# Kernel tuning notes

Measured on AMD Instinct MI355X. Metric: run time of the kernel, lower is better.

Reference implementation:

```python
import jax, jax.numpy as jnp
import numpy as np

K = 8               # top-k frequencies
PRED_LEN = 96       # prediction_length
LOW_FREQ = 1        # low_frequency cutoff (drops DC)


def setup_inputs() -> dict:
    key = jax.random.key(0)
    x = jax.random.normal(key, (32, 2048, 64), dtype=jnp.float32)
    return {"x": x}


def reference(x):
    b, t, d = x.shape
    x_freq = jnp.fft.rfft(x, axis=1)                 # (b, t//2+1, d) complex
    freqs = jnp.fft.rfftfreq(t).astype(x.dtype)
    if t % 2 == 0:
        x_freq = x_freq[:, LOW_FREQ:-1]              # drop DC and Nyquist
        f = freqs[LOW_FREQ:-1]
    else:
        x_freq = x_freq[:, LOW_FREQ:]
        f = freqs[LOW_FREQ:]

    # top-k over frequency dim (axis=1), independently per (b, d)
    mag = jnp.abs(x_freq)                            # (b, F, d)
    _, idx = jax.lax.top_k(jnp.moveaxis(mag, 1, 2), K)  # (b, d, K), sorted desc
    idx = jnp.moveaxis(idx, 1, 2)                    # (b, K, d)
    x_k = jnp.take_along_axis(x_freq, idx, axis=1)   # (b, K, d) complex
    f_k = f[idx]                                     # (b, K, d)

    # extrapolate: add conjugate (negative) frequencies, then cos-sum
    x2 = jnp.concatenate([x_k, jnp.conj(x_k)], axis=1)  # (b, 2K, d)
    f2 = jnp.concatenate([f_k, -f_k], axis=1)           # (b, 2K, d)
    t_val = jnp.arange(t + PRED_LEN, dtype=x.dtype)     # (T,)
    amp = jnp.abs(x2) / t                               # (b, 2K, d)
    phase = jnp.angle(x2)                               # (b, 2K, d)
    # (b, 2K, T, d) broadcast intermediate, reduced over freq axis
    x_time = amp[:, :, None, :] * jnp.cos(
        2.0 * np.float32(np.pi) * f2[:, :, None, :] * t_val[None, None, :, None]
        + phase[:, :, None, :]
    )
    return x_time.sum(axis=1)                        # (b, t+PRED_LEN, d)
```

## Files before the change

### kernel.cpp

```cpp
#include <hip/hip_runtime.h>
#include <math.h>

#define BB 32
#define TT 2048
#define DD 64
#define PRED 96
#define TP (TT + PRED)
#define KTOP 8
#define MARGIN 1e-4f
#define PI_D 3.14159265358979323846

__device__ __forceinline__ int br6(int l) { return (int)(__brev((unsigned)l) >> 26); }
static constexpr int BR4[16] = {0,8,4,12,2,10,6,14,1,9,5,13,3,11,7,15};
static constexpr float C32T[16] = {
    1.0f, 0.98078528040323044913f, 0.92387953251128675613f, 0.83146961230254523708f,
    0.70710678118654752440f, 0.55557023301960222474f, 0.38268343236508977173f, 0.19509032201612826785f,
    0.0f, -0.19509032201612826785f, -0.38268343236508977173f, -0.55557023301960222474f,
    -0.70710678118654752440f, -0.83146961230254523708f, -0.92387953251128675613f, -0.98078528040323044913f};
static constexpr float S32T[16] = {
    0.0f, 0.19509032201612826785f, 0.38268343236508977173f, 0.55557023301960222474f,
    0.70710678118654752440f, 0.83146961230254523708f, 0.92387953251128675613f, 0.98078528040323044913f,
    1.0f, 0.98078528040323044913f, 0.92387953251128675613f, 0.83146961230254523708f,
    0.70710678118654752440f, 0.55557023301960222474f, 0.38268343236508977173f, 0.19509032201612826785f};

__device__ __forceinline__ float2 ctw(float2 a, int m) {
    const float rev = (float)m * (1.0f / 2048.0f);
    const float c = __builtin_amdgcn_cosf(rev);
    const float s = __builtin_amdgcn_sinf(rev);
    return make_float2(a.x * c + a.y * s, a.y * c - a.x * s);
}

#define SG(wi,pi,ii) POOL[(wi) * 2176 + (pi) * 34 + 2 * (ii)]
#define SRE(pr,a) POOL[9216 + (pr) * 4224 + (a)]
#define SIM(pr,a) POOL[9216 + (pr) * 4224 + 2112 + (a)]

__global__ __launch_bounds__(256, 2) void fused_kernel(const float* __restrict__ x,
                                                       float* __restrict__ out) {
    __shared__ float POOL[17664];
    __shared__ int   coefK[4][KTOP];
    __shared__ float coefR[4][KTOP], coefI[4][KTOP];

    const int t    = threadIdx.x;
    const int wv   = t >> 6, p = t & 63;
    const int pair = wv >> 1, w = wv & 1;
    const int bid  = blockIdx.x;
    const int xcd  = bid & 7;
    const int idx  = bid >> 3;
    const int b    = (idx >> 3) * 4 + (xcd >> 1);
    const int grp4 = (xcd & 1) * 8 + (idx & 7);
    const int dp   = grp4 * 2 + pair;
    const int ch   = grp4 * 4 + wv;

    const int rl = 2 * br6(p) + w;

    float2 v[16];
    if (wv < 2) {
        const float4* xq = (const float4*)x;
        const size_t rowbase = (size_t)b * TT;
        #pragma unroll
        for (int i = 0; i < 16; ++i) {
            const int n = 128 * BR4[i] + rl;
            const float4 f = xq[(rowbase + (size_t)n) * 16 + grp4];
            v[i] = make_float2(f.x, f.y);
            *(float2*)&SG(wv, p, i) = make_float2(f.z, f.w);
        }
    }
    __syncthreads();
    if (wv >= 2) {
        #pragma unroll
        for (int i = 0; i < 16; ++i)
            v[i] = *(const float2*)&SG(w, p, i);
    }
    __syncthreads();

    #pragma unroll
    for (int s = 1; s <= 4; ++s) {
        const int m = 1 << s, half = m >> 1, stepw = 32 >> s;
        #pragma unroll
        for (int g = 0; g < 16; g += m) {
            #pragma unroll
            for (int j = 0; j < half; ++j) {
                const float c = C32T[j * stepw], sn = S32T[j * stepw];
                const int i0 = g + j, i1 = i0 + half;
                const float tr = c * v[i1].x + sn * v[i1].y;
                const float ti = c * v[i1].y - sn * v[i1].x;
                v[i1] = make_float2(v[i0].x - tr, v[i0].y - ti);
                v[i0] = make_float2(v[i0].x + tr, v[i0].y + ti);
            }
        }
    }

    #pragma unroll
    for (int q = 1; q < 16; ++q) v[q] = ctw(v[q], (rl * q) & (TT - 1));

    #pragma unroll
    for (int s = 1; s <= 6; ++s) {
        const int half = 1 << (s - 1);
        const float rev = (float)(p & (half - 1)) / (float)(1 << s);
        const float wc  = __builtin_amdgcn_cosf(rev);
        const float wsn = __builtin_amdgcn_sinf(rev);
        const bool  hi  = (p & half) != 0;
        #pragma unroll
        for (int q = 0; q < 16; ++q) {
            float2 pv;
            pv.x = __shfl_xor(v[q].x, half, 64);
            pv.y = __shfl_xor(v[q].y, half, 64);
            const float2 bsv = hi ? v[q] : pv;
            const float2 asv = hi ? pv : v[q];
            const float tr = wc * bsv.x + wsn * bsv.y;
            const float ti = wc * bsv.y - wsn * bsv.x;
            v[q] = hi ? make_float2(asv.x - tr, asv.y - ti)
                      : make_float2(asv.x + tr, asv.y + ti);
        }
    }

    {
        const int exw = pair * 4608 + w * 2304 + p * 36;
        #pragma unroll
        for (int c = 0; c < 8; ++c)
            *(float4*)&POOL[exw + 4 * c] =
                make_float4(v[2*c].x, v[2*c].y, v[2*c+1].x, v[2*c+1].y);
    }
    __syncthreads();
    {
        const int exr = pair * 4608 + (1 - w) * 2304 + p * 36;
        const float revp = (float)p * (1.0f / 128.0f);
        const float wc7 = __builtin_amdgcn_cosf(revp);
        const float ws7 = __builtin_amdgcn_sinf(revp);
        const int kb = 1024 * w + 16 * p;
        #pragma unroll
        for (int c = 0; c < 8; ++c) {
            const float4 g = *(const float4*)&POOL[exr + 4 * c];
            #pragma unroll
            for (int e = 0; e < 2; ++e) {
                const int q = 2 * c + e;
                const float2 pv = e ? make_float2(g.z, g.w) : make_float2(g.x, g.y);
                const float2 bsv = w ? v[q] : pv;
                const float2 asv = w ? pv : v[q];
                const float tr = wc7 * bsv.x + ws7 * bsv.y;
                const float ti = wc7 * bsv.y - ws7 * bsv.x;
                const int k = kb + q, a = k + (k >> 5);
                SRE(pair, a) = w ? (asv.x - tr) : (asv.x + tr);
                SIM(pair, a) = w ? (asv.y - ti) : (asv.y + ti);
            }
        }
    }
    __syncthreads();

    unsigned A[16];
    #pragma unroll
    for (int q = 0; q < 16; ++q) {
        const int k = 16 * p + q;
        unsigned kk = 0u;
        if (k != 0) {
            const int a1 = k + (k >> 5);
            const int pk = TT - k, a2 = pk + (pk >> 5);
            const float zr = SRE(pair, a1), zi = SIM(pair, a1);
            const float yr = SRE(pair, a2), yi = SIM(pair, a2);
            float cr, ci;
            if (w == 0) { cr = 0.5f * (zr + yr); ci = 0.5f * (zi - yi); }
            else        { cr = 0.5f * (zi + yi); ci = 0.5f * (yr - zr); }
            const float mg = cr * cr + ci * ci;
            kk = (__float_as_uint(mg) & 0xFFFFF800u) | (unsigned)(2047 - k);
        }
        A[q] = kk;
    }

    #pragma unroll
    for (int sz = 2; sz <= 16; sz <<= 1) {
        #pragma unroll
        for (int d = sz >> 1; d > 0; d >>= 1) {
            #pragma unroll
            for (int i2 = 0; i2 < 16; ++i2) {
                const int j2i = i2 ^ d;
                if (j2i > i2) {
                    const bool desc = ((i2 & sz) == 0);
                    const unsigned a = A[i2], b2 = A[j2i];
                    const unsigned mx = a > b2 ? a : b2, mn = a > b2 ? b2 : a;
                    A[i2] = desc ? mx : mn;  A[j2i] = desc ? mn : mx;
                }
            }
        }
    }
    #pragma unroll
    for (int off = 1; off <= 32; off <<= 1) {
        unsigned Bv[16];
        #pragma unroll
        for (int i2 = 0; i2 < 16; ++i2)
            Bv[i2] = (unsigned)__shfl_xor((int)A[i2], off, 64);
        #pragma unroll
        for (int i2 = 0; i2 < 16; ++i2) {
            const unsigned o = Bv[15 - i2];
            A[i2] = A[i2] > o ? A[i2] : o;
        }
        #pragma unroll
        for (int d = 8; d > 0; d >>= 1) {
            #pragma unroll
            for (int i2 = 0; i2 < 16; ++i2) {
                if ((i2 & d) == 0) {
                    const int j2i = i2 + d;
                    const unsigned a = A[i2], b2 = A[j2i];
                    A[i2] = a > b2 ? a : b2;  A[j2i] = a > b2 ? b2 : a;
                }
            }
        }
    }

    const float m8f = __uint_as_float(A[7] & 0xFFFFF800u);
    unsigned bandmask = 0u;
    #pragma unroll
    for (int r = 0; r < 16; ++r) {
        const float mr = __uint_as_float(A[r] & 0xFFFFF800u);
        if (fabsf(mr - m8f) <= MARGIN * m8f) bandmask |= (1u << r);
    }
    const int flg = (bandmask != (1u << 7)) ? 1 : 0;

    unsigned myk = 0u;
    #pragma unroll
    for (int i2 = 0; i2 < 16; ++i2) myk = (p == i2) ? A[i2] : myk;
    const int kcand = 2047 - (int)(myk & 0x7FFu);

    if (!flg && p < KTOP) {
        const int k = kcand, a1 = k + (k >> 5), pk = TT - k, a2 = pk + (pk >> 5);
        const float zr = SRE(pair, a1), zi = SIM(pair, a1);
        const float yr = SRE(pair, a2), yi = SIM(pair, a2);
        float cr, ci;
        if (w == 0) { cr = 0.5f * (zr + yr); ci = 0.5f * (zi - yi); }
        else        { cr = 0.5f * (zi + yi); ci = 0.5f * (yr - zr); }
        coefK[wv][p] = k;
        coefR[wv][p] = cr * (2.0f / (float)TT);
        coefI[wv][p] = ci * (2.0f / (float)TT);
    }

    if (flg) {
        float sv[32];
        const float* xs = x + (size_t)b * TT * DD + ch;
        #pragma unroll
        for (int m2 = 0; m2 < 32; ++m2)
            sv[m2] = xs[(size_t)(p + 64 * m2) * DD];
        const double thA = -2.0 * PI_D * (double)p / 64.0;
        const double thB = -2.0 * PI_D * (double)p / (double)TT;
        const double wac = cos(thA), was = sin(thA);
        const double wbc = cos(thB), wbs = sin(thB);

        const unsigned bm = bandmask;
        const int lo = (int)__builtin_ctz(bm);
        double myM = 0.0, myR = 0.0, myI = 0.0;
        for (int r = 0; r < 16; ++r) {
            if (!((bm >> r) & 1u)) continue;
            const int kr = __shfl(kcand, r, 64);
            double ar = 0.0, ai = 0.0;
            for (int m2 = 0; m2 < 32; ++m2) {
                const int n  = p + 64 * m2;
                const int mm = (n * kr) & (TT - 1);
                const double qc  = __shfl(wac, mm >> 5, 64);
                const double qs  = __shfl(was, mm >> 5, 64);
                const double rc2 = __shfl(wbc, mm & 31, 64);
                const double rs2 = __shfl(wbs, mm & 31, 64);
                const double wr = qc * rc2 - qs * rs2;
                const double wi = qc * rs2 + qs * rc2;
                ar = fma((double)sv[m2], wr, ar);
                ai = fma((double)sv[m2], wi, ai);
            }
            #pragma unroll
            for (int off = 32; off; off >>= 1) {
                ar += __shfl_xor(ar, off, 64);
                ai += __shfl_xor(ai, off, 64);
            }
            if (p == r) { myM = ar * ar + ai * ai; myR = ar; myI = ai; }
        }
        const int h16 = p & 15;
        const double selfM = __shfl(myM, h16, 64);
        const int    selfK = __shfl(kcand, h16, 64);
        int rb = 0;
        for (int r2 = 0; r2 < 16; ++r2) {
            if (!((bm >> r2) & 1u)) continue;
            const double om = __shfl(myM, r2, 64);
            const int    ok = __shfl(kcand, r2, 64);
            if (r2 != h16 && (om > selfM || (om == selfM && ok < selfK))) ++rb;
        }
        const int isband = (int)((bm >> h16) & 1u);
        const int rank = isband ? (lo + rb) : h16;
        if (p < 16 && rank < KTOP) {
            coefK[wv][rank] = kcand;
            if (isband) {
                coefR[wv][rank] = (float)(myR * (2.0 / (double)TT));
                coefI[wv][rank] = (float)(myI * (2.0 / (double)TT));
            } else {
                const int k = kcand, a1 = k + (k >> 5), pk = TT - k, a2 = pk + (pk >> 5);
                const float zr = SRE(pair, a1), zi = SIM(pair, a1);
                const float yr = SRE(pair, a2), yi = SIM(pair, a2);
                float cr, ci;
                if (w == 0) { cr = 0.5f * (zr + yr); ci = 0.5f * (zi - yi); }
                else        { cr = 0.5f * (zi + yi); ci = 0.5f * (yr - zr); }
                coefR[wv][rank] = cr * (2.0f / (float)TT);
                coefI[wv][rank] = ci * (2.0f / (float)TT);
            }
        }
    }
    __syncthreads();

    const int d4 = t & 3, tq = t >> 2;
    int   kc[KTOP];
    float fr[KTOP], fi[KTOP], pc[KTOP], ps[KTOP], rc[KTOP], rs[KTOP];
    #pragma unroll
    for (int pp = 0; pp < KTOP; ++pp) {
        kc[pp] = coefK[d4][pp];
        fr[pp] = coefR[d4][pp];
        fi[pp] = coefI[d4][pp];
        const int j0 = (kc[pp] * tq) & (TT - 1);
        const float rv0 = (float)j0 * (1.0f / 2048.0f);
        pc[pp] = __builtin_amdgcn_cosf(rv0);
        ps[pp] = __builtin_amdgcn_sinf(rv0);
        const int jr = (kc[pp] * 64) & (TT - 1);
        const float rvr = (float)jr * (1.0f / 2048.0f);
        rc[pp] = __builtin_amdgcn_cosf(rvr);
        rs[pp] = __builtin_amdgcn_sinf(rvr);
    }
    float* ob = out + (size_t)b * TP * DD + grp4 * 4 + d4;
    #pragma unroll 2
    for (int m = 0; m < 34; ++m) {
        const int tv = tq + 64 * m;
        float acc = 0.0f;
        #pragma unroll
        for (int pp = 0; pp < KTOP; ++pp) acc += fr[pp] * pc[pp] - fi[pp] * ps[pp];
        if (tv < TP) ob[(size_t)tv * DD] = acc;
        #pragma unroll
        for (int pp = 0; pp < KTOP; ++pp) {
            const float nc = pc[pp] * rc[pp] - ps[pp] * rs[pp];
            const float ns = pc[pp] * rs[pp] + ps[pp] * rc[pp];
            pc[pp] = nc; ps[pp] = ns;
        }
    }
}

extern "C" void kernel_launch(void* const* d_in, const int* in_sizes, int n_in,
                              void* d_out, int out_size, void* d_ws, size_t ws_size,
                              hipStream_t stream) {
    const float* x = (const float*)d_in[0];
    float* out = (float*)d_out;
    (void)d_ws; (void)ws_size; (void)in_sizes; (void)n_in; (void)out_size;

    fused_kernel<<<BB * 16, 256, 0, stream>>>(x, out);
}
```

Measured before the change: 92.91 us.

## Replace cross-lane shuffles with DPP/permlane swaps and drop a barrier

Cross-lane exchanges in the FFT butterfly stages and the top-k bitonic merge now use DPP row operations for xor-1/xor-2 and permlane16/32 swap builtins for xor-16/32, replacing ds_bpermute-based shuffles that go through LDS hardware. The first butterfly stage is specialised with trivial twiddles. The staging buffer is moved to a separate LDS region, which lets one __syncthreads after the initial load be removed. The intent is lower latency for cross-lane data movement and fewer barriers, at the cost of relying on gfx950-specific builtins, with shuffle fallbacks when they are unavailable.

```diff
diff --git a/kernel.cpp b/kernel.cpp
--- a/kernel.cpp
+++ b/kernel.cpp
@@ -30,7 +30,72 @@
     return make_float2(a.x * c + a.y * s, a.y * c - a.x * s);
 }
 
-#define SG(wi,pi,ii) POOL[(wi) * 2176 + (pi) * 34 + 2 * (ii)]
+typedef unsigned uint2e __attribute__((ext_vector_type(2)));
+
+#if __has_builtin(__builtin_amdgcn_permlane16_swap)
+#define HAS_PL16 1
+#else
+#define HAS_PL16 0
+#endif
+#if __has_builtin(__builtin_amdgcn_permlane32_swap)
+#define HAS_PL32 1
+#else
+#define HAS_PL32 0
+#endif
+
+__device__ __forceinline__ float dpp_xor1f(float x) {
+    return __int_as_float(__builtin_amdgcn_update_dpp(
+        __float_as_int(x), __float_as_int(x), 0xB1 ,
+        0xF, 0xF, false));
+}
+__device__ __forceinline__ float dpp_xor2f(float x) {
+    return __int_as_float(__builtin_amdgcn_update_dpp(
+        __float_as_int(x), __float_as_int(x), 0x4E ,
+        0xF, 0xF, false));
+}
+__device__ __forceinline__ void lohi16f(float xv, bool isHi, float& lo, float& hi) {
+#if HAS_PL16
+    (void)isHi;
+    uint2e r = __builtin_amdgcn_permlane16_swap(__float_as_uint(xv),
+                                                __float_as_uint(xv), false, false);
+    lo = __uint_as_float(r[0]); hi = __uint_as_float(r[1]);
+#else
+    const float o = __shfl_xor(xv, 16, 64);
+    lo = isHi ? o : xv; hi = isHi ? xv : o;
+#endif
+}
+__device__ __forceinline__ void lohi32f(float xv, bool isHi, float& lo, float& hi) {
+#if HAS_PL32
+    (void)isHi;
+    uint2e r = __builtin_amdgcn_permlane32_swap(__float_as_uint(xv),
+                                                __float_as_uint(xv), false, false);
+    lo = __uint_as_float(r[0]); hi = __uint_as_float(r[1]);
+#else
+    const float o = __shfl_xor(xv, 32, 64);
+    lo = isHi ? o : xv; hi = isHi ? xv : o;
+#endif
+}
+__device__ __forceinline__ unsigned sel_partner(unsigned xv, int off, int p) {
+    if (off == 1)
+        return (unsigned)__builtin_amdgcn_update_dpp((int)xv, (int)xv, 0xB1, 0xF, 0xF, false);
+    if (off == 2)
+        return (unsigned)__builtin_amdgcn_update_dpp((int)xv, (int)xv, 0x4E, 0xF, 0xF, false);
+#if HAS_PL16
+    if (off == 16) {
+        uint2e r = __builtin_amdgcn_permlane16_swap(xv, xv, false, false);
+        return (p & 16) ? r[0] : r[1];
+    }
+#endif
+#if HAS_PL32
+    if (off == 32) {
+        uint2e r = __builtin_amdgcn_permlane32_swap(xv, xv, false, false);
+        return (p & 32) ? r[0] : r[1];
+    }
+#endif
+    return (unsigned)__shfl_xor((int)xv, off, 64);
+}
+
+#define SG(wi,pi,ii) POOL[9216 + (wi) * 2176 + (pi) * 34 + 2 * (ii)]
 #define SRE(pr,a) POOL[9216 + (pr) * 4224 + (a)]
 #define SIM(pr,a) POOL[9216 + (pr) * 4224 + 2112 + (a)]
 
@@ -48,7 +113,6 @@
     const int idx  = bid >> 3;
     const int b    = (idx >> 3) * 4 + (xcd >> 1);
     const int grp4 = (xcd & 1) * 8 + (idx & 7);
-    const int dp   = grp4 * 2 + pair;
     const int ch   = grp4 * 4 + wv;
 
     const int rl = 2 * br6(p) + w;
@@ -71,7 +135,6 @@
         for (int i = 0; i < 16; ++i)
             v[i] = *(const float2*)&SG(w, p, i);
     }
-    __syncthreads();
 
     #pragma unroll
     for (int s = 1; s <= 4; ++s) {
@@ -93,8 +156,35 @@
     #pragma unroll
     for (int q = 1; q < 16; ++q) v[q] = ctw(v[q], (rl * q) & (TT - 1));
 
-    #pragma unroll
-    for (int s = 1; s <= 6; ++s) {
+    {
+        const bool hi = (p & 1) != 0;
+        #pragma unroll
+        for (int q = 0; q < 16; ++q) {
+            float2 pv;
+            pv.x = dpp_xor1f(v[q].x); pv.y = dpp_xor1f(v[q].y);
+            v[q].x = hi ? (pv.x - v[q].x) : (v[q].x + pv.x);
+            v[q].y = hi ? (pv.y - v[q].y) : (v[q].y + pv.y);
+        }
+    }
+    {
+        const float rev = (float)(p & 1) * 0.25f;
+        const float wc  = __builtin_amdgcn_cosf(rev);
+        const float wsn = __builtin_amdgcn_sinf(rev);
+        const bool  hi  = (p & 2) != 0;
+        #pragma unroll
+        for (int q = 0; q < 16; ++q) {
+            float2 pv;
+            pv.x = dpp_xor2f(v[q].x); pv.y = dpp_xor2f(v[q].y);
+            const float2 bsv = hi ? v[q] : pv;
+            const float2 asv = hi ? pv : v[q];
+            const float tr = wc * bsv.x + wsn * bsv.y;
+            const float ti = wc * bsv.y - wsn * bsv.x;
+            v[q] = hi ? make_float2(asv.x - tr, asv.y - ti)
+                      : make_float2(asv.x + tr, asv.y + ti);
+        }
+    }
+    #pragma unroll
+    for (int s = 3; s <= 4; ++s) {
         const int half = 1 << (s - 1);
         const float rev = (float)(p & (half - 1)) / (float)(1 << s);
         const float wc  = __builtin_amdgcn_cosf(rev);
@@ -111,6 +201,38 @@
             const float ti = wc * bsv.y - wsn * bsv.x;
             v[q] = hi ? make_float2(asv.x - tr, asv.y - ti)
                       : make_float2(asv.x + tr, asv.y + ti);
+        }
+    }
+    {
+        const float rev = (float)(p & 15) * (1.0f / 32.0f);
+        const float wc  = __builtin_amdgcn_cosf(rev);
+        const float wsn = __builtin_amdgcn_sinf(rev);
+        const bool  hi  = (p & 16) != 0;
+        #pragma unroll
+        for (int q = 0; q < 16; ++q) {
+            float lox, hix, loy, hiy;
+            lohi16f(v[q].x, hi, lox, hix);
+            lohi16f(v[q].y, hi, loy, hiy);
+            const float tr = wc * hix + wsn * hiy;
+            const float ti = wc * hiy - wsn * hix;
+            v[q].x = hi ? (lox - tr) : (lox + tr);
+            v[q].y = hi ? (loy - ti) : (loy + ti);
+        }
+    }
+    {
+        const float rev = (float)(p & 31) * (1.0f / 64.0f);
+        const float wc  = __builtin_amdgcn_cosf(rev);
+        const float wsn = __builtin_amdgcn_sinf(rev);
+        const bool  hi  = (p & 32) != 0;
+        #pragma unroll
+        for (int q = 0; q < 16; ++q) {
+            float lox, hix, loy, hiy;
+            lohi32f(v[q].x, hi, lox, hix);
+            lohi32f(v[q].y, hi, loy, hiy);
+            const float tr = wc * hix + wsn * hiy;
+            const float ti = wc * hiy - wsn * hix;
+            v[q].x = hi ? (lox - tr) : (lox + tr);
+            v[q].y = hi ? (loy - ti) : (loy + ti);
         }
     }
 
@@ -187,7 +309,7 @@
         unsigned Bv[16];
         #pragma unroll
         for (int i2 = 0; i2 < 16; ++i2)
-            Bv[i2] = (unsigned)__shfl_xor((int)A[i2], off, 64);
+            Bv[i2] = sel_partner(A[i2], off, p);
         #pragma unroll
         for (int i2 = 0; i2 < 16; ++i2) {
             const unsigned o = Bv[15 - i2];
@@ -317,7 +439,8 @@
         rc[pp] = __builtin_amdgcn_cosf(rvr);
         rs[pp] = __builtin_amdgcn_sinf(rvr);
     }
-    float* ob = out + (size_t)b * TP * DD + grp4 * 4 + d4;
+    const int grp4b = grp4;
+    float* ob = out + (size_t)b * TP * DD + grp4b * 4 + d4;
     #pragma unroll 2
     for (int m = 0; m < 34; ++m) {
         const int tv = tq + 64 * m;
```

Measured after the change: 94.33 us. No clear change (+1.5%).
